# Performance work log

Measured on AMD Instinct MI355X. Metric: run time of the kernel, lower is better.

The kernel has to match this reference:

```python
import jax, jax.numpy as jnp
import numpy as np

M, N, T = 32, 32, 512
H1 = (M + N) * 10 * 8      # 5120
H2 = M * N * 4             # 4096
HID = 1000                 # GRU hidden (hardcoded in module)
EPS = 1e-12


def _l2norm(x):
    # torch.nn.functional.normalize: x / max(||x||_2, eps)
    return x / jnp.maximum(jnp.linalg.norm(x), EPS)


def setup_inputs() -> dict:
    key = jax.random.key(0)
    ks = jax.random.split(key, 16)
    rn = lambda k, shp, s: (jax.random.normal(k, shp, dtype=jnp.float32) * s)
    inp = {
        "y": rn(ks[0], (T, N), 1.0),
        "F": rn(ks[1], (M, M), 0.5 / np.sqrt(M)),   # stable dynamics
        "H": rn(ks[2], (N, M), 1.0 / np.sqrt(M)),
        "m1x0": rn(ks[3], (M,), 1.0),
        "h0": rn(ks[4], (HID,), 1.0),
        "W1": rn(ks[5], (H1, M + N), 1.0 / np.sqrt(M + N)),
        "b1": rn(ks[6], (H1,), 0.01),
        "Wih": rn(ks[7], (3 * HID, H1), 1.0 / np.sqrt(H1)),
        "bih": rn(ks[8], (3 * HID,), 0.01),
        "Whh": rn(ks[9], (3 * HID, HID), 1.0 / np.sqrt(HID)),
        "bhh": rn(ks[10], (3 * HID,), 0.01),
        "W2": rn(ks[11], (H2, HID), 1.0 / np.sqrt(HID)),
        "b2": rn(ks[12], (H2,), 0.01),
        "W3": rn(ks[13], (M * N, H2), 1.0 / np.sqrt(H2)),
        "b3": rn(ks[14], (M * N,), 0.01),
    }
    return inp


def reference(y, F, H, m1x0, h0, W1, b1, Wih, bih, Whh, bhh, W2, b2, W3, b3):
    m, n = F.shape[0], H.shape[0]

    def step(carry, yt):
        m1x_prior, m1x_post, h = carry
        # step_prior
        m1x_prev_prior = m1x_prior
        m1x_prior = F @ m1x_post              # [m]
        m1y = H @ m1x_prior                   # [n]
        # step_KGain_est: features
        dm1x_n = _l2norm(m1x_post - m1x_prev_prior)
        dm1y_n = _l2norm(yt - m1y)
        kin = jnp.concatenate([dm1y_n, dm1x_n])  # [n+m]
        # KGain_step: Linear+ReLU -> single-step GRU -> Linear+ReLU -> Linear
        x = jax.nn.relu(W1 @ kin + b1)        # [H1]
        gi = Wih @ x + bih                    # [3*HID]
        gh = Whh @ h + bhh
        ir, iz, ic = jnp.split(gi, 3)
        hr, hz, hc = jnp.split(gh, 3)
        r = jax.nn.sigmoid(ir + hr)
        z = jax.nn.sigmoid(iz + hz)
        c = jnp.tanh(ic + r * hc)
        h_new = (1.0 - z) * c + z * h         # GRU hidden [HID]
        l2 = jax.nn.relu(W2 @ h_new + b2)     # [H2]
        KG = (W3 @ l2 + b3).reshape(m, n)     # Kalman gain
        # KNet_step: innovation update
        m1x_post_new = m1x_prior + KG @ (yt - m1y)
        return (m1x_prior, m1x_post_new, h_new), m1x_post_new

    init = (m1x0, m1x0, h0)
    _, posts = jax.lax.scan(step, init, y)
    return posts  # [T, m]
```

## Files before the change

### kernel.cpp

```cpp
#include <hip/hip_runtime.h>
#include <cmath>

#define Mdim 32
#define Ndim 32
#define Tsteps 512
#define H1dim 5120
#define H2dim 4096
#define HIDdim 1000
#define NWG 256
#define NTHR 1024
#define POLLER 320

typedef unsigned int u32;
typedef unsigned short u16;

__device__ u16 g_w2b[H2dim * HIDdim];
__device__ u16 g_w3t[H2dim * Mdim * Ndim];

#define OFF_WIH 0
#define OFF_WHH 122880
#define OFF_UNION 146880
#define OFF_H9 157120
#define OFF_MISC 161640
#define SMEM_BYTES 162560

#define MI_POST 0
#define MI_PRIOR 32
#define MI_INNOV 96
#define MI_KIN 128
#define MI_GI 192
#define MI_GH 204

__device__ __forceinline__ u16 f2bf(float f) {
  u32 u = __float_as_uint(f);
  return (u16)((u + 0x7fffu + ((u >> 16) & 1u)) >> 16);
}
__device__ __forceinline__ float bflo(u32 u) { return __uint_as_float(u << 16); }
__device__ __forceinline__ float bfhi(u32 u) { return __uint_as_float(u & 0xffff0000u); }

__device__ __forceinline__ float dot4(float4 a, float4 b) {
  return a.x * b.x + a.y * b.y + a.z * b.z + a.w * b.w;
}
__device__ __forceinline__ float dot8_bb(uint4 a, uint4 b) {
  float s = 0.f;
  s = fmaf(bflo(a.x), bflo(b.x), s); s = fmaf(bfhi(a.x), bfhi(b.x), s);
  s = fmaf(bflo(a.y), bflo(b.y), s); s = fmaf(bfhi(a.y), bfhi(b.y), s);
  s = fmaf(bflo(a.z), bflo(b.z), s); s = fmaf(bfhi(a.z), bfhi(b.z), s);
  s = fmaf(bflo(a.w), bflo(b.w), s); s = fmaf(bfhi(a.w), bfhi(b.w), s);
  return s;
}
__device__ __forceinline__ float dot8_bf(uint4 a, const float* x8) {
  float s = 0.f;
  s = fmaf(bflo(a.x), x8[0], s); s = fmaf(bfhi(a.x), x8[1], s);
  s = fmaf(bflo(a.y), x8[2], s); s = fmaf(bfhi(a.y), x8[3], s);
  s = fmaf(bflo(a.z), x8[4], s); s = fmaf(bfhi(a.z), x8[5], s);
  s = fmaf(bflo(a.w), x8[6], s); s = fmaf(bfhi(a.w), x8[7], s);
  return s;
}

__device__ __forceinline__ float wave_reduce64(float v) {
#pragma unroll
  for (int off = 32; off >= 1; off >>= 1) v += __shfl_xor(v, off, 64);
  return v;
}
__device__ __forceinline__ float group16_reduce(float v) {
#pragma unroll
  for (int off = 8; off >= 1; off >>= 1) v += __shfl_xor(v, off, 64);
  return v;
}

__device__ __forceinline__ float4 ldg_cg4(const float* p) {
  float4 r;
  asm volatile("global_load_dwordx4 %0, %1, off sc0 sc1\n\ts_waitcnt vmcnt(0)"
               : "=v"(r) : "v"(p) : "memory");
  return r;
}
__device__ __forceinline__ uint4 ldg_cg4u(const void* p) {
  uint4 r;
  asm volatile("global_load_dwordx4 %0, %1, off sc0 sc1\n\ts_waitcnt vmcnt(0)"
               : "=v"(r) : "v"(p) : "memory");
  return r;
}
__device__ __forceinline__ void ldg2_cg4(const float* p0, const float* p1,
                                         float4& r0, float4& r1) {
  asm volatile("global_load_dwordx4 %0, %2, off sc0 sc1\n\t"
               "global_load_dwordx4 %1, %3, off sc0 sc1\n\t"
               "s_waitcnt vmcnt(0)"
               : "=&v"(r0), "=&v"(r1) : "v"(p0), "v"(p1) : "memory");
}
__device__ __forceinline__ void stg_cg1(float* p, float v) {
  asm volatile("global_store_dword %0, %1, off sc0 sc1" :: "v"(p), "v"(v) : "memory");
}
__device__ __forceinline__ void stg_cg_u16(u16* p, u16 v) {
  u32 vv = v;
  asm volatile("global_store_short %0, %1, off sc0 sc1" :: "v"(p), "v"(vv) : "memory");
}

__device__ __forceinline__ void gb_arrive(u32* bar) {
  asm volatile("s_waitcnt vmcnt(0)" ::: "memory");
  __syncthreads();
  if (threadIdx.x == POLLER) {
    u32 g = (u32)blockIdx.x & 15u;
    u32 a = __hip_atomic_fetch_add(bar + g * 16, 1u, __ATOMIC_RELAXED,
                                   __HIP_MEMORY_SCOPE_AGENT);
    if ((a & 15u) == 15u) {
      u32 b = __hip_atomic_fetch_add(bar + 256, 1u, __ATOMIC_RELAXED,
                                     __HIP_MEMORY_SCOPE_AGENT);
      if ((b & 15u) == 15u)
        __hip_atomic_fetch_add(bar + 320, 1u, __ATOMIC_RELAXED,
                               __HIP_MEMORY_SCOPE_AGENT);
    }
  }
}
__device__ __forceinline__ void gb_wait(u32* bar, u32 nb) {
  if (threadIdx.x == POLLER) {
    while (__hip_atomic_load(bar + 320, __ATOMIC_RELAXED,
                             __HIP_MEMORY_SCOPE_AGENT) < nb)
      __builtin_amdgcn_s_sleep(2);
  }
  __syncthreads();
}

__global__ void convert_w2(const float* __restrict__ W2) {
  int i = blockIdx.x * 1024 + threadIdx.x;
  if (i < H2dim * HIDdim) g_w2b[i] = f2bf(W2[i]);
}

__global__ void convert_w3t(const float* __restrict__ W3) {
  __shared__ float tile[32][33];
  int tr = blockIdx.x >> 7;
  int tc = blockIdx.x & 127;
  int r0 = tr * 32, c0 = tc * 32;
  int j = threadIdx.x & 31, i0 = threadIdx.x >> 5;
#pragma unroll
  for (int p = 0; p < 4; ++p) {
    int i = i0 + p * 8;
    tile[i][j] = W3[(size_t)(r0 + i) * H2dim + c0 + j];
  }
  __syncthreads();
#pragma unroll
  for (int p = 0; p < 4; ++p) {
    int i = i0 + p * 8;
    g_w3t[(size_t)(c0 + i) * 1024 + r0 + j] = f2bf(tile[j][i]);
  }
}

__global__ void __launch_bounds__(NTHR)
knet_kernel(const float* __restrict__ y, const float* __restrict__ F,
            const float* __restrict__ Hm, const float* __restrict__ m1x0,
            const float* __restrict__ h0, const float* __restrict__ W1,
            const float* __restrict__ b1, const float* __restrict__ Wih,
            const float* __restrict__ bih, const float* __restrict__ Whh,
            const float* __restrict__ bhh, const float* __restrict__ b2,
            const float* __restrict__ b3, float* __restrict__ out,
            u32* bar, u16* xb, float* hbuf, float* dpart) {
  extern __shared__ char smem[];
  u16* s_wih = (u16*)(smem + OFF_WIH);
  u16* s_whh = (u16*)(smem + OFF_WHH);
  u16* s_x = (u16*)(smem + OFF_UNION);
  float4* s_red4 = (float4*)(smem + OFF_UNION);
  float* s_redf = (float*)(smem + OFF_UNION);
  float* s_pd = (float*)(smem + OFF_UNION);
  float* s_h9 = (float*)(smem + OFF_H9);
  float* s_m = (float*)(smem + OFF_MISC);
  float* s_post = s_m + MI_POST;
  float* s_prior = s_m + MI_PRIOR;
  float* s_innov = s_m + MI_INNOV;
  float* s_kin = s_m + MI_KIN;
  float* s_gi = s_m + MI_GI;
  float* s_gh = s_m + MI_GH;

  const int tid = threadIdx.x;
  const int w = tid >> 6;
  const int lane = tid & 63;
  const int wg = blockIdx.x;
  const int k0 = wg * 4;
  const bool gru_wg = (wg < 250);
  u32 nb = 0;

  if (gru_wg) {
#pragma unroll 1
    for (int r = 0; r < 12; ++r) {
      const float* src = Wih + (size_t)((r >> 2) * HIDdim + k0 + (r & 3)) * H1dim;
      u16* dst = s_wih + r * H1dim;
      for (int e = tid; e < H1dim; e += NTHR) dst[e] = f2bf(src[e]);
    }
#pragma unroll 1
    for (int r = 0; r < 12; ++r) {
      const float* src = Whh + (size_t)((r >> 2) * HIDdim + k0 + (r & 3)) * HIDdim;
      u16* dst = s_whh + r * HIDdim;
      for (int e = tid; e < HIDdim; e += NTHR) dst[e] = f2bf(src[e]);
    }
  }
  if (tid < 250) {
    float4 hv = ((const float4*)h0)[tid];
    int b0 = tid * 4;
    s_h9[((b0 + 0) >> 3) * 9 + ((b0 + 0) & 7)] = hv.x;
    s_h9[((b0 + 1) >> 3) * 9 + ((b0 + 1) & 7)] = hv.y;
    s_h9[((b0 + 2) >> 3) * 9 + ((b0 + 2) & 7)] = hv.z;
    s_h9[((b0 + 3) >> 3) * 9 + ((b0 + 3) & 7)] = hv.w;
  }
  __syncthreads();

  const int c2 = wg * 16 + w;
  const int w1row = wg * 20 + w * 4 + (lane >> 4);
  float prior = 0.f, bb = 0.f, yv = 0.f;
  if (w == 0 && lane < 32) {
    prior = m1x0[lane];
    yv = y[lane];
  }

  auto gh_compute = [&]() {
    int base = (w - 12) * 3;
#pragma unroll
    for (int rr = 0; rr < 3; ++rr) {
      int r = base + rr;
      const uint4* wr = (const uint4*)(s_whh + r * HIDdim);
      float acc = dot8_bf(wr[lane], s_h9 + lane * 9);
      if (lane < 61) acc += dot8_bf(wr[lane + 64], s_h9 + (lane + 64) * 9);
      acc = wave_reduce64(acc);
      if (lane == 0) s_gh[r] = acc + bhh[(r >> 2) * HIDdim + k0 + (r & 3)];
    }
  };
  if (gru_wg && w >= 12) gh_compute();

  for (int t = 0; t < Tsteps; ++t) {
    if (t > 0) {
      float4 a0, a1;
      ldg2_cg4(dpart + tid * 4, dpart + (tid + 1024) * 4, a0, a1);
      float4 s;
      s.x = a0.x + a1.x; s.y = a0.y + a1.y; s.z = a0.z + a1.z; s.w = a0.w + a1.w;
#pragma unroll
      for (int off = 8; off <= 32; off <<= 1) {
        s.x += __shfl_xor(s.x, off, 64);
        s.y += __shfl_xor(s.y, off, 64);
        s.z += __shfl_xor(s.z, off, 64);
        s.w += __shfl_xor(s.w, off, 64);
      }
      if (lane < 8) s_red4[w * 8 + lane] = s;
    }
    __syncthreads();
    if (w == 0) {
      float p = 0.f, inn = 0.f;
      float prev = prior;
      if (lane < 32) {
        if (t == 0) {
          p = m1x0[lane];
        } else {
          float dsum = 0.f;
#pragma unroll
          for (int ww = 0; ww < 16; ++ww) dsum += s_redf[ww * 32 + lane];
          p = prior + dsum + bb;
          if (wg == 0) out[(t - 1) * Mdim + lane] = p;
        }
        s_post[lane] = p;
      }
      asm volatile("" ::: "memory");
      if (lane < 32) {
        const float4* Fr = (const float4*)(F + lane * Mdim);
        const float4* pp = (const float4*)s_post;
        float s = 0.f;
#pragma unroll
        for (int j = 0; j < 8; ++j) s += dot4(Fr[j], pp[j]);
        prior = s;
        s_prior[lane] = s;
      }
      asm volatile("" ::: "memory");
      if (lane < 32) {
        const float4* Hr = (const float4*)(Hm + lane * Mdim);
        const float4* pp = (const float4*)s_prior;
        float s = 0.f;
#pragma unroll
        for (int j = 0; j < 8; ++j) s += dot4(Hr[j], pp[j]);
        inn = yv - s;
        s_innov[lane] = inn;
      }
      float vd = __shfl(p, lane & 31, 64) - __shfl(prev, lane & 31, 64);
      float v = (lane < 32) ? inn : vd;
      float sq = v * v;
#pragma unroll
      for (int off = 16; off >= 1; off >>= 1) sq += __shfl_xor(sq, off, 32);
      s_kin[lane] = v / fmaxf(sqrtf(sq), 1e-12f);
    }
    __syncthreads();
    if (w < 5) {
      float s = dot4(((const float4*)W1)[w1row * 16 + (lane & 15)],
                     ((const float4*)s_kin)[lane & 15]);
      s = group16_reduce(s);
      if ((lane & 15) == 0) stg_cg_u16(xb + w1row, f2bf(fmaxf(s + b1[w1row], 0.f)));
    }
    ++nb;
    gb_arrive(bar);
    gb_wait(bar, nb);

    if (gru_wg) {
      if (tid < 640) ((uint4*)s_x)[tid] = ldg_cg4u((const char*)xb + tid * 16);
      __syncthreads();
      if (w < 12) {
        const uint4* wr = (const uint4*)(s_wih + w * H1dim);
        const uint4* xr = (const uint4*)s_x;
        float acc = 0.f;
#pragma unroll
        for (int i = 0; i < 10; ++i) {
          int j = lane + 64 * i;
          acc += dot8_bb(wr[j], xr[j]);
        }
        acc = wave_reduce64(acc);
        if (lane == 0) s_gi[w] = acc + bih[(w >> 2) * HIDdim + k0 + (w & 3)];
      }
      __syncthreads();
      if (tid < 4) {
        int k = k0 + tid;
        float hold = s_h9[(k >> 3) * 9 + (k & 7)];
        float ir = s_gi[tid], iz = s_gi[4 + tid], ic = s_gi[8 + tid];
        float r = 1.f / (1.f + expf(-(ir + s_gh[tid])));
        float z = 1.f / (1.f + expf(-(iz + s_gh[4 + tid])));
        float c_ = tanhf(ic + r * s_gh[8 + tid]);
        stg_cg1(hbuf + k, (1.f - z) * c_ + z * hold);
      }
    }
    ++nb;
    gb_arrive(bar);
    float u;
    uint4 w2a, w2b_;
    {
      const uint4* tr3 = (const uint4*)(g_w3t + (size_t)c2 * 1024);
      uint4 t0 = tr3[2 * lane], t1 = tr3[2 * lane + 1];
      const float* iv = s_innov + 16 * (lane & 1);
      u = dot8_bf(t0, iv) + dot8_bf(t1, iv + 8);
      u += __shfl_xor(u, 1, 64);
      const uint4* w2p = (const uint4*)(g_w2b + (size_t)c2 * HIDdim);
      w2a = w2p[lane];
      w2b_ = (lane < 61) ? w2p[lane + 64] : make_uint4(0u, 0u, 0u, 0u);
    }
    gb_wait(bar, nb);

    if (tid < 250) {
      float4 hv = ldg_cg4(hbuf + tid * 4);
      int b0 = tid * 4;
      s_h9[((b0 + 0) >> 3) * 9 + ((b0 + 0) & 7)] = hv.x;
      s_h9[((b0 + 1) >> 3) * 9 + ((b0 + 1) & 7)] = hv.y;
      s_h9[((b0 + 2) >> 3) * 9 + ((b0 + 2) & 7)] = hv.z;
      s_h9[((b0 + 3) >> 3) * 9 + ((b0 + 3) & 7)] = hv.w;
    }
    __syncthreads();
    {
      float acc = dot8_bf(w2a, s_h9 + lane * 9);
      if (lane < 61) acc += dot8_bf(w2b_, s_h9 + (lane + 64) * 9);
      acc = wave_reduce64(acc);
      float l2c = fmaxf(acc + b2[c2], 0.f);
      if ((lane & 1) == 0) s_pd[w * 32 + (lane >> 1)] = l2c * u;
    }
    __syncthreads();
    if (tid < 32) {
      float pdv = 0.f;
#pragma unroll
      for (int ww = 0; ww < 16; ++ww) pdv += s_pd[ww * 32 + tid];
      stg_cg1(dpart + wg * 32 + tid, pdv);
    }
    ++nb;
    gb_arrive(bar);
    if (gru_wg && w >= 12) gh_compute();
    if (w == 0 && lane < 32) {
      int tn = (t + 1 < Tsteps) ? t + 1 : Tsteps - 1;
      yv = y[tn * Ndim + lane];
      float b = 0.f;
#pragma unroll 8
      for (int j = 0; j < 32; ++j) b = fmaf(b3[lane * 32 + j], s_innov[j], b);
      bb = b;
    }
    gb_wait(bar, nb);
  }

  if (wg == 0) {
    float4 a0, a1;
    ldg2_cg4(dpart + tid * 4, dpart + (tid + 1024) * 4, a0, a1);
    float4 s;
    s.x = a0.x + a1.x; s.y = a0.y + a1.y; s.z = a0.z + a1.z; s.w = a0.w + a1.w;
#pragma unroll
    for (int off = 8; off <= 32; off <<= 1) {
      s.x += __shfl_xor(s.x, off, 64);
      s.y += __shfl_xor(s.y, off, 64);
      s.z += __shfl_xor(s.z, off, 64);
      s.w += __shfl_xor(s.w, off, 64);
    }
    if (lane < 8) s_red4[w * 8 + lane] = s;
    __syncthreads();
    if (w == 0 && lane < 32) {
      float d = 0.f;
#pragma unroll
      for (int ww = 0; ww < 16; ++ww) d += s_redf[ww * 32 + lane];
      out[(Tsteps - 1) * Mdim + lane] = prior + d + bb;
    }
  }
}

extern "C" void kernel_launch(void* const* d_in, const int* in_sizes, int n_in,
                              void* d_out, int out_size, void* d_ws, size_t ws_size,
                              hipStream_t stream) {
  const float* y    = (const float*)d_in[0];
  const float* F    = (const float*)d_in[1];
  const float* Hm   = (const float*)d_in[2];
  const float* m1x0 = (const float*)d_in[3];
  const float* h0   = (const float*)d_in[4];
  const float* W1   = (const float*)d_in[5];
  const float* b1   = (const float*)d_in[6];
  const float* Wih  = (const float*)d_in[7];
  const float* bih  = (const float*)d_in[8];
  const float* Whh  = (const float*)d_in[9];
  const float* bhh  = (const float*)d_in[10];
  const float* W2   = (const float*)d_in[11];
  const float* b2   = (const float*)d_in[12];
  const float* W3   = (const float*)d_in[13];
  const float* b3   = (const float*)d_in[14];
  float* out = (float*)d_out;

  u32* bar   = (u32*)d_ws;
  u16* xb    = (u16*)((char*)d_ws + 4096);
  float* hbuf  = (float*)((char*)d_ws + 14336);
  float* dpart = (float*)((char*)d_ws + 18432);

  convert_w2<<<4000, 1024, 0, stream>>>(W2);
  convert_w3t<<<4096, 256, 0, stream>>>(W3);
  hipMemsetAsync(d_ws, 0, 4096, stream);
  hipFuncSetAttribute((const void*)knet_kernel,
                      hipFuncAttributeMaxDynamicSharedMemorySize, SMEM_BYTES);
  void* args[] = {&y, &F, &Hm, &m1x0, &h0, &W1, &b1, &Wih, &bih, &Whh, &bhh,
                  &b2, &b3, &out, &bar, &xb, &hbuf, &dpart};
  hipLaunchCooperativeKernel((const void*)knet_kernel, dim3(NWG), dim3(NTHR),
                             args, SMEM_BYTES, stream);
}
```

Measured before the change: 6.417 ms.

## Replace two grid barriers with per-element step-tagged flag polling

```diff
diff --git a/kernel.cpp b/kernel.cpp
--- a/kernel.cpp
+++ b/kernel.cpp
@@ -13,6 +13,7 @@
 
 typedef unsigned int u32;
 typedef unsigned short u16;
+typedef unsigned int u32x4 __attribute__((ext_vector_type(4)));
 
 __device__ u16 g_w2b[H2dim * HIDdim];
 __device__ u16 g_w3t[H2dim * Mdim * Ndim];
@@ -63,18 +64,7 @@
   for (int off = 32; off >= 1; off >>= 1) v += __shfl_xor(v, off, 64);
   return v;
 }
-__device__ __forceinline__ float group16_reduce(float v) {
-#pragma unroll
-  for (int off = 8; off >= 1; off >>= 1) v += __shfl_xor(v, off, 64);
-  return v;
-}
-
-__device__ __forceinline__ float4 ldg_cg4(const float* p) {
-  float4 r;
-  asm volatile("global_load_dwordx4 %0, %1, off sc0 sc1\n\ts_waitcnt vmcnt(0)"
-               : "=v"(r) : "v"(p) : "memory");
-  return r;
-}
+
 __device__ __forceinline__ uint4 ldg_cg4u(const void* p) {
   uint4 r;
   asm volatile("global_load_dwordx4 %0, %1, off sc0 sc1\n\ts_waitcnt vmcnt(0)"
@@ -91,9 +81,9 @@
 __device__ __forceinline__ void stg_cg1(float* p, float v) {
   asm volatile("global_store_dword %0, %1, off sc0 sc1" :: "v"(p), "v"(v) : "memory");
 }
-__device__ __forceinline__ void stg_cg_u16(u16* p, u16 v) {
-  u32 vv = v;
-  asm volatile("global_store_short %0, %1, off sc0 sc1" :: "v"(p), "v"(vv) : "memory");
+__device__ __forceinline__ void stg_cg4u(void* p, u32 a, u32 b, u32 c, u32 d) {
+  u32x4 v; v.x = a; v.y = b; v.z = c; v.w = d;
+  asm volatile("global_store_dwordx4 %0, %1, off sc0 sc1" :: "v"(p), "v"(v) : "memory");
 }
 
 __device__ __forceinline__ void gb_arrive(u32* bar) {
@@ -153,7 +143,7 @@
             const float* __restrict__ bih, const float* __restrict__ Whh,
             const float* __restrict__ bhh, const float* __restrict__ b2,
             const float* __restrict__ b3, float* __restrict__ out,
-            u32* bar, u16* xb, float* hbuf, float* dpart) {
+            u32* bar, u32* xbt, u32* hbt, float* dpart) {
   extern __shared__ char smem[];
   u16* s_wih = (u16*)(smem + OFF_WIH);
   u16* s_whh = (u16*)(smem + OFF_WHH);
@@ -203,7 +193,6 @@
   __syncthreads();
 
   const int c2 = wg * 16 + w;
-  const int w1row = wg * 20 + w * 4 + (lane >> 4);
   float prior = 0.f, bb = 0.f, yv = 0.f;
   if (w == 0 && lane < 32) {
     prior = m1x0[lane];
@@ -225,6 +214,7 @@
   if (gru_wg && w >= 12) gh_compute();
 
   for (int t = 0; t < Tsteps; ++t) {
+    const u32 want = (u32)(t + 1);
     if (t > 0) {
       float4 a0, a1;
       ldg2_cg4(dpart + tid * 4, dpart + (tid + 1024) * 4, a0, a1);
@@ -283,44 +273,38 @@
       s_kin[lane] = v / fmaxf(sqrtf(sq), 1e-12f);
     }
     __syncthreads();
-    if (w < 5) {
-      float s = dot4(((const float4*)W1)[w1row * 16 + (lane & 15)],
-                     ((const float4*)s_kin)[lane & 15]);
-      s = group16_reduce(s);
-      if ((lane & 15) == 0) stg_cg_u16(xb + w1row, f2bf(fmaxf(s + b1[w1row], 0.f)));
-    }
-    ++nb;
-    gb_arrive(bar);
-    gb_wait(bar, nb);
-
-    if (gru_wg) {
-      if (tid < 640) ((uint4*)s_x)[tid] = ldg_cg4u((const char*)xb + tid * 16);
-      __syncthreads();
-      if (w < 12) {
-        const uint4* wr = (const uint4*)(s_wih + w * H1dim);
-        const uint4* xr = (const uint4*)s_x;
-        float acc = 0.f;
-#pragma unroll
-        for (int i = 0; i < 10; ++i) {
-          int j = lane + 64 * i;
-          acc += dot8_bb(wr[j], xr[j]);
-        }
-        acc = wave_reduce64(acc);
-        if (lane == 0) s_gi[w] = acc + bih[(w >> 2) * HIDdim + k0 + (w & 3)];
-      }
-      __syncthreads();
-      if (tid < 4) {
-        int k = k0 + tid;
-        float hold = s_h9[(k >> 3) * 9 + (k & 7)];
-        float ir = s_gi[tid], iz = s_gi[4 + tid], ic = s_gi[8 + tid];
-        float r = 1.f / (1.f + expf(-(ir + s_gh[tid])));
-        float z = 1.f / (1.f + expf(-(iz + s_gh[4 + tid])));
-        float c_ = tanhf(ic + r * s_gh[8 + tid]);
-        stg_cg1(hbuf + k, (1.f - z) * c_ + z * hold);
-      }
-    }
-    ++nb;
-    gb_arrive(bar);
+
+    if (w == 0) {
+      int r = lane / 3;
+      int p = lane - r * 3;
+      float acc = 0.f;
+      if (r < 20) {
+        const float4* Wr = (const float4*)W1 + (size_t)(wg * 20 + r) * 16;
+        const float4* kc = (const float4*)s_kin;
+#pragma unroll
+        for (int c = p; c < 16; c += 3) acc += dot4(Wr[c], kc[c]);
+      }
+      int rr = (r < 20) ? r : 0;
+      float a1v = __shfl(acc, rr * 3 + 1, 64);
+      float a2v = __shfl(acc, rr * 3 + 2, 64);
+      u32 myval = 0;
+      if (r < 20 && p == 0)
+        myval = (u32)f2bf(fmaxf(acc + a1v + a2v + b1[wg * 20 + r], 0.f));
+      u32 vs[7];
+      int q = (lane < 3) ? lane : 0;
+#pragma unroll
+      for (int s2 = 0; s2 < 7; ++s2) {
+        int ridx = q * 7 + s2;
+        vs[s2] = __shfl(myval, (ridx < 20 ? ridx : 0) * 3, 64);
+      }
+      if (lane < 3) {
+        stg_cg4u((char*)xbt + (size_t)(wg * 3 + lane) * 16,
+                 vs[0] | (vs[1] << 16),
+                 vs[2] | (vs[3] << 16),
+                 vs[4] | (vs[5] << 16),
+                 ((lane == 2) ? 0u : vs[6]) | (want << 16));
+      }
+    }
     float u;
     uint4 w2a, w2b_;
     {
@@ -333,17 +317,65 @@
       w2a = w2p[lane];
       w2b_ = (lane < 61) ? w2p[lane + 64] : make_uint4(0u, 0u, 0u, 0u);
     }
-    gb_wait(bar, nb);
-
-    if (tid < 250) {
-      float4 hv = ldg_cg4(hbuf + tid * 4);
-      int b0 = tid * 4;
-      s_h9[((b0 + 0) >> 3) * 9 + ((b0 + 0) & 7)] = hv.x;
-      s_h9[((b0 + 1) >> 3) * 9 + ((b0 + 1) & 7)] = hv.y;
-      s_h9[((b0 + 2) >> 3) * 9 + ((b0 + 2) & 7)] = hv.z;
-      s_h9[((b0 + 3) >> 3) * 9 + ((b0 + 3) & 7)] = hv.w;
-    }
-    __syncthreads();
+    if (gru_wg && tid >= 256) {
+      int g = tid - 256;
+      int swg = g / 3;
+      int q = g - swg * 3;
+      const char* gp = (const char*)xbt + (size_t)g * 16;
+      uint4 v;
+      for (;;) {
+        v = ldg_cg4u(gp);
+        if ((v.w >> 16) == want) break;
+        __builtin_amdgcn_s_sleep(1);
+      }
+      u16* sx = (u16*)s_x;
+      int base = swg * 20 + q * 7;
+      sx[base + 0] = (u16)(v.x & 0xffff);
+      sx[base + 1] = (u16)(v.x >> 16);
+      sx[base + 2] = (u16)(v.y & 0xffff);
+      sx[base + 3] = (u16)(v.y >> 16);
+      sx[base + 4] = (u16)(v.z & 0xffff);
+      sx[base + 5] = (u16)(v.z >> 16);
+      if (q != 2) sx[base + 6] = (u16)(v.w & 0xffff);
+    }
+    __syncthreads();
+
+    if (gru_wg && w < 12) {
+      const uint4* wr = (const uint4*)(s_wih + w * H1dim);
+      const uint4* xr = (const uint4*)s_x;
+      float acc = 0.f;
+#pragma unroll
+      for (int i = 0; i < 10; ++i) {
+        int j = lane + 64 * i;
+        acc += dot8_bb(wr[j], xr[j]);
+      }
+      acc = wave_reduce64(acc);
+      if (lane == 0) s_gi[w] = acc + bih[(w >> 2) * HIDdim + k0 + (w & 3)];
+    }
+    __syncthreads();
+
+    if (gru_wg && w == 0 && lane < 4) {
+      int k = k0 + lane;
+      float hold = s_h9[(k >> 3) * 9 + (k & 7)];
+      float ir = s_gi[lane], iz = s_gi[4 + lane], ic = s_gi[8 + lane];
+      float r = 1.f / (1.f + expf(-(ir + s_gh[lane])));
+      float z = 1.f / (1.f + expf(-(iz + s_gh[4 + lane])));
+      float c_ = tanhf(ic + r * s_gh[8 + lane]);
+      float hv = (1.f - z) * c_ + z * hold;
+      stg_cg4u((char*)hbt + (size_t)k * 16, __float_as_uint(hv), want, 0u, 0u);
+    }
+    if (tid < HIDdim) {
+      const char* gp = (const char*)hbt + (size_t)tid * 16;
+      uint4 v;
+      for (;;) {
+        v = ldg_cg4u(gp);
+        if (v.y == want) break;
+        __builtin_amdgcn_s_sleep(1);
+      }
+      s_h9[(tid >> 3) * 9 + (tid & 7)] = __uint_as_float(v.x);
+    }
+    __syncthreads();
+
     {
       float acc = dot8_bf(w2a, s_h9 + lane * 9);
       if (lane < 61) acc += dot8_bf(w2b_, s_h9 + (lane + 64) * 9);
@@ -416,17 +448,17 @@
   float* out = (float*)d_out;
 
   u32* bar   = (u32*)d_ws;
-  u16* xb    = (u16*)((char*)d_ws + 4096);
-  float* hbuf  = (float*)((char*)d_ws + 14336);
-  float* dpart = (float*)((char*)d_ws + 18432);
+  u32* xbt   = (u32*)((char*)d_ws + 4096);
+  u32* hbt   = (u32*)((char*)d_ws + 16384);
+  float* dpart = (float*)((char*)d_ws + 32768);
 
   convert_w2<<<4000, 1024, 0, stream>>>(W2);
   convert_w3t<<<4096, 256, 0, stream>>>(W3);
-  hipMemsetAsync(d_ws, 0, 4096, stream);
+  hipMemsetAsync(d_ws, 0, 32768, stream);
   hipFuncSetAttribute((const void*)knet_kernel,
                       hipFuncAttributeMaxDynamicSharedMemorySize, SMEM_BYTES);
   void* args[] = {&y, &F, &Hm, &m1x0, &h0, &W1, &b1, &Wih, &bih, &Whh, &bhh,
-                  &b2, &b3, &out, &bar, &xb, &hbuf, &dpart};
+                  &b2, &b3, &out, &bar, &xbt, &hbt, &dpart};
   hipLaunchCooperativeKernel((const void*)knet_kernel, dim3(NWG), dim3(NTHR),
                              args, SMEM_BYTES, stream);
 }
```

Measured after the change: 6.385 ms. Within noise of the previous version (-0.5%).
